# Performance work log

Hardware: AMD Instinct MI355X
Metric: run time of the kernel (lower is better)

The kernel has to match this reference:

```python
import jax, jax.numpy as jnp
import numpy as np

N, IN_F, OUT_F, H = 4096, 256, 64, 8

def setup_inputs() -> dict:
    key = jax.random.key(0)
    k1, k2, k3, k4 = jax.random.split(key, 4)
    x = jax.random.normal(k1, (N, IN_F), dtype=jnp.float32)
    adj = jax.random.randint(k2, (N, N), 0, 2, dtype=jnp.int32)
    # Xavier-uniform-ish init scale for params
    W = jax.random.uniform(k3, (H, IN_F, OUT_F), dtype=jnp.float32, minval=-1.0, maxval=1.0) * np.sqrt(6.0 / (IN_F + OUT_F))
    a = jax.random.uniform(k4, (H, 2 * OUT_F, 1), dtype=jnp.float32, minval=-1.0, maxval=1.0) * np.sqrt(6.0 / (2 * OUT_F + 1))
    return {"x": x, "adj": adj, "W": W, "a": a}

def reference(x, adj, W, a):
    # h: (H, N, F) per-head projected features
    h = jnp.einsum('nf,hfo->hno', x, W)
    F = h.shape[-1]
    # Decompose concat-score: [h_i || h_j] @ a == h_i @ a[:F] + h_j @ a[F:]
    a_src = a[:, :F, 0]   # (H, F)
    a_dst = a[:, F:, 0]   # (H, F)
    src = jnp.einsum('hno,ho->hn', h, a_src)  # (H, N)
    dst = jnp.einsum('hno,ho->hn', h, a_dst)  # (H, N)
    e = jax.nn.leaky_relu(src[:, :, None] + dst[:, None, :], negative_slope=0.2)  # (H, N, N)
    e = jnp.where(adj[None, :, :] == 0, -jnp.inf, e)
    alpha = jax.nn.softmax(e, axis=2)  # dropout is identity at eval
    h_prime = jnp.einsum('hnm,hmo->hno', alpha, h).mean(axis=0)  # (N, F)
    return jax.nn.elu(h_prime)
```

## Files before the change

kernel.cpp:

```cpp
#include <hip/hip_runtime.h>
#include <hip/hip_fp16.h>
#include <cstdint>

#define N_NODES 4096
#define IN_FEAT 256
#define OUT_FEAT 64
#define NHEAD 8
#define LOG2E 1.4426950408889634f

typedef _Float16 f16;
typedef f16   f16x2 __attribute__((ext_vector_type(2)));
typedef f16   f16x8 __attribute__((ext_vector_type(8)));
typedef float f32x4 __attribute__((ext_vector_type(4)));

#define OFF_SRCPK 4194304
#define OFF_DSTE1 4325376
#define OFF_DSTE5 4390912
#define OFF_EM    4718592
#define OFF_NUMA  21495808ULL
#define OFF_DENA  29884416ULL

union HU { unsigned u; f16x2 h; };
union A8 { f16x8 v; unsigned u[4]; };

__device__ __forceinline__ void async_copy16(const void* g, void* l) {
    __builtin_amdgcn_global_load_lds(
        (const __attribute__((address_space(1))) void*)g,
        (__attribute__((address_space(3))) void*)l, 16, 0, 0);
}

static __device__ inline unsigned pkh2(float a, float b) {
    union { f16 h[2]; unsigned u; } t;
    t.h[0] = (f16)a; t.h[1] = (f16)b; return t.u;
}

__global__ __launch_bounds__(256, 4) void gat_prep(
    const int*   __restrict__ adj,
    unsigned*    __restrict__ em32,
    float*       __restrict__ zeroBase,
    const float* __restrict__ x,
    const float* __restrict__ W,
    const float* __restrict__ a,
    f16*      __restrict__ h_t,
    unsigned* __restrict__ srcPK,
    f16*      __restrict__ dstE1,
    f16*      __restrict__ dstE5)
{
    __shared__ f16 xs[16][264];

    if (blockIdx.x >= 1536) {
        size_t off = ((size_t)(blockIdx.x - 1536) * 256 + threadIdx.x) * 8;
        float4 z = {0.f, 0.f, 0.f, 0.f};
        *(float4*)(zeroBase + off)     = z;
        *(float4*)(zeroBase + off + 4) = z;
        return;
    }
    if (blockIdx.x >= 512) {
        const int bi   = blockIdx.x - 512;
        const int wv   = threadIdx.x >> 6;
        const int lane = threadIdx.x & 63;
        const int row  = bi * 4 + wv;
        const int* p   = adj + (size_t)row * N_NODES;
        unsigned* dst  = em32 + (size_t)row * (N_NODES / 4);
        #pragma unroll 4
        for (int s = 0; s < 16; ++s) {
            int4 v = *(const int4*)(p + s * 256 + lane * 4);
            unsigned d = (v.x ? 0x000000FFu : 0u) | (v.y ? 0x0000FF00u : 0u)
                       | (v.z ? 0x00FF0000u : 0u) | (v.w ? 0xFF000000u : 0u);
            dst[s * 64 + lane] = d;
        }
        return;
    }

    const int lane = threadIdx.x & 63;
    const int wv   = threadIdx.x >> 6;
    const int tile = blockIdx.x >> 1;
    const int hd   = (blockIdx.x & 1) * 4 + wv;
    const int r    = lane & 15;
    const int q    = lane >> 4;
    const int nb   = tile * 16;

    #pragma unroll
    for (int c = 0; c < 4; ++c) {
        int idx = c * 1024 + threadIdx.x * 4;
        int row = idx >> 8, col = idx & 255;
        float4 v = *(const float4*)(x + (size_t)(nb + row) * IN_FEAT + col);
        uint2 st = { pkh2(v.x, v.y), pkh2(v.z, v.w) };
        *(uint2*)(&xs[row][col]) = st;
    }
    __syncthreads();

    const float* Wg = W + (size_t)hd * (IN_FEAT * OUT_FEAT);
    f32x4 acc[4] = {};

    #pragma unroll 2
    for (int k0 = 0; k0 < IN_FEAT; k0 += 32) {
        f16x8 af = *(const f16x8*)(&xs[r][k0 + q * 8]);
        #pragma unroll
        for (int f = 0; f < 4; ++f) {
            f16x8 bf;
            #pragma unroll
            for (int j = 0; j < 8; ++j)
                bf[j] = (f16)Wg[(size_t)(k0 + q * 8 + j) * OUT_FEAT + 16 * f + r];
            acc[f] = __builtin_amdgcn_mfma_f32_16x16x32_f16(af, bf, acc[f], 0, 0, 0);
        }
    }

    float asv[4], adv[4];
    #pragma unroll
    for (int f = 0; f < 4; ++f) {
        asv[f] = a[hd * 128 + 16 * f + r];
        adv[f] = a[hd * 128 + 64 + 16 * f + r];
    }
    float sp[4], dp[4];
    #pragma unroll
    for (int reg = 0; reg < 4; ++reg) {
        sp[reg] = acc[0][reg] * asv[0] + acc[1][reg] * asv[1]
                + acc[2][reg] * asv[2] + acc[3][reg] * asv[3];
        dp[reg] = acc[0][reg] * adv[0] + acc[1][reg] * adv[1]
                + acc[2][reg] * adv[2] + acc[3][reg] * adv[3];
    }
    #pragma unroll
    for (int m = 1; m <= 8; m <<= 1) {
        #pragma unroll
        for (int reg = 0; reg < 4; ++reg) {
            sp[reg] += __shfl_xor(sp[reg], m);
            dp[reg] += __shfl_xor(dp[reg], m);
        }
    }

    #pragma unroll
    for (int f = 0; f < 4; ++f) {
        uint2 st = { pkh2(acc[f][0], acc[f][1]), pkh2(acc[f][2], acc[f][3]) };
        *(uint2*)(h_t + (size_t)(hd * OUT_FEAT + 16 * f + r) * N_NODES + nb + 4 * q) = st;
    }

    if (r == 0) {
        #pragma unroll
        for (int reg = 0; reg < 4; ++reg) {
            int row = nb + 4 * q + reg;
            float s = sp[reg] * LOG2E;
            float d = dp[reg] * LOG2E;
            srcPK[hd * N_NODES + row] = pkh2(exp2f(s), exp2f(0.2f * s));
            dstE1[hd * N_NODES + row] = (f16)exp2f(d);
            dstE5[hd * N_NODES + row] = (f16)exp2f(0.2f * d);
        }
    }
}

__global__ __launch_bounds__(256, 4) void gat_phase2p(
    const f16* __restrict__ h_t,
    const unsigned* __restrict__ srcPK,
    const f16* __restrict__ dstE1,
    const f16* __restrict__ dstE5,
    const unsigned char* __restrict__ emask8,
    float* __restrict__ numA,
    float* __restrict__ denA)
{
    __shared__ f16 Vbuf[2][8320];

    const int t    = threadIdx.x;
    const int lane = t & 63;
    const int wv   = t >> 6;
    const int r    = lane & 15;
    const int q    = lane >> 4;
    const int q8   = q * 8;

    const int hd     = blockIdx.x >> 7;
    const int rowgrp = (blockIdx.x >> 2) & 31;
    const int chunk  = blockIdx.x & 3;
    const int nblk   = rowgrp * 128;
    const int n0     = nblk + wv * 32;
    const int mbase  = chunk * 1024;

    HU s0u, s1u;
    s0u.u = srcPK[hd * N_NODES + n0 + r];
    s1u.u = srcPK[hd * N_NODES + n0 + 16 + r];
    const f16x2 se1_0 = { s0u.h[0], s0u.h[0] };
    const f16x2 se5_0 = { s0u.h[1], s0u.h[1] };
    const f16x2 se1_1 = { s1u.h[0], s1u.h[0] };
    const f16x2 se5_1 = { s1u.h[1], s1u.h[1] };

    const f16* Vhead = h_t + (size_t)hd * OUT_FEAT * N_NODES + mbase;
    const f16* srcV  = Vhead + (size_t)(t >> 2) * N_NODES + (t & 3) * 8;
    const unsigned char* srcM =
        emask8 + (size_t)(nblk + (t >> 1)) * N_NODES + mbase + (t & 1) * 16;
    const f16* ebase = ((t >> 2) & 1) ? dstE5 : dstE1;
    const f16* esrc  = ebase + (size_t)hd * N_NODES + mbase
                             + (t >> 3) * 32 + (t & 3) * 8;

    f32x4 acc0 = {}, acc1 = {}, acc2 = {}, acc3 = {}, accD0 = {};
    f32x4 acc4 = {}, acc5 = {}, acc6 = {}, acc7 = {}, accD1 = {};
    f16x8 ones;
    #pragma unroll
    for (int j = 0; j < 8; ++j) ones[j] = (f16)1.0f;

    auto stage = [&](int buf, int it) {
        const int c64 = it * 64;
        async_copy16(srcV + c64,      &Vbuf[buf][t * 8]);
        async_copy16(srcV + c64 + 32, &Vbuf[buf][2048 + t * 8]);
        async_copy16(srcM + c64,      &Vbuf[buf][4096 + t * 8]);
        async_copy16(srcM + c64 + 32, &Vbuf[buf][6144 + t * 8]);
        if (t < 16) async_copy16(esrc + c64, &Vbuf[buf][8192 + t * 8]);
    };

    stage(0, 0);

    for (int it = 0; it < 16; ++it) {
        const int cur = it & 1;
        __syncthreads();

        stage(1 - cur, (it + 1) & 15);

        #pragma unroll
        for (int s = 0; s < 2; ++s) {
            const int vb = s * 2048;
            uint4 e1v = *(const uint4*)(&Vbuf[cur][8192 + s * 64 + q8]);
            uint4 e5v = *(const uint4*)(&Vbuf[cur][8224 + s * 64 + q8]);
            uint2 m0v = *(const uint2*)(&Vbuf[cur][4096 + s * 2048 + (wv * 32 + r) * 16 + q * 4]);
            uint2 m1v = *(const uint2*)(&Vbuf[cur][4096 + s * 2048 + (wv * 32 + 16 + r) * 16 + q * 4]);

            unsigned e1d[4] = {e1v.x, e1v.y, e1v.z, e1v.w};
            unsigned e5d[4] = {e5v.x, e5v.y, e5v.z, e5v.w};
            unsigned mk0[4], mk1[4];
            mk0[0] = __builtin_amdgcn_perm(0u, m0v.x, 0x01010000u);
            mk0[1] = __builtin_amdgcn_perm(0u, m0v.x, 0x03030202u);
            mk0[2] = __builtin_amdgcn_perm(0u, m0v.y, 0x01010000u);
            mk0[3] = __builtin_amdgcn_perm(0u, m0v.y, 0x03030202u);
            mk1[0] = __builtin_amdgcn_perm(0u, m1v.x, 0x01010000u);
            mk1[1] = __builtin_amdgcn_perm(0u, m1v.x, 0x03030202u);
            mk1[2] = __builtin_amdgcn_perm(0u, m1v.y, 0x01010000u);
            mk1[3] = __builtin_amdgcn_perm(0u, m1v.y, 0x03030202u);

            A8 A0, A1;
            #pragma unroll
            for (int jp = 0; jp < 4; ++jp) {
                HU ed1; ed1.u = e1d[jp];
                HU ed5; ed5.u = e5d[jp];
                HU w0, w1;
                w0.h = __builtin_elementwise_max(se1_0 * ed1.h, se5_0 * ed5.h);
                w1.h = __builtin_elementwise_max(se1_1 * ed1.h, se5_1 * ed5.h);
                A0.u[jp] = w0.u & mk0[jp];
                A1.u[jp] = w1.u & mk1[jp];
            }

            f16x8 b0 = *(const f16x8*)(&Vbuf[cur][vb + (     r) * 32 + q8]);
            f16x8 b1 = *(const f16x8*)(&Vbuf[cur][vb + (16 + r) * 32 + q8]);
            f16x8 b2 = *(const f16x8*)(&Vbuf[cur][vb + (32 + r) * 32 + q8]);
            f16x8 b3 = *(const f16x8*)(&Vbuf[cur][vb + (48 + r) * 32 + q8]);

            acc0  = __builtin_amdgcn_mfma_f32_16x16x32_f16(A0.v, b0,   acc0,  0, 0, 0);
            acc1  = __builtin_amdgcn_mfma_f32_16x16x32_f16(A0.v, b1,   acc1,  0, 0, 0);
            acc2  = __builtin_amdgcn_mfma_f32_16x16x32_f16(A0.v, b2,   acc2,  0, 0, 0);
            acc3  = __builtin_amdgcn_mfma_f32_16x16x32_f16(A0.v, b3,   acc3,  0, 0, 0);
            accD0 = __builtin_amdgcn_mfma_f32_16x16x32_f16(A0.v, ones, accD0, 0, 0, 0);
            acc4  = __builtin_amdgcn_mfma_f32_16x16x32_f16(A1.v, b0,   acc4,  0, 0, 0);
            acc5  = __builtin_amdgcn_mfma_f32_16x16x32_f16(A1.v, b1,   acc5,  0, 0, 0);
            acc6  = __builtin_amdgcn_mfma_f32_16x16x32_f16(A1.v, b2,   acc6,  0, 0, 0);
            acc7  = __builtin_amdgcn_mfma_f32_16x16x32_f16(A1.v, b3,   acc7,  0, 0, 0);
            accD1 = __builtin_amdgcn_mfma_f32_16x16x32_f16(A1.v, ones, accD1, 0, 0, 0);
        }
    }

    #pragma unroll
    for (int reg = 0; reg < 4; ++reg) {
        int row0 = n0 + 4 * q + reg;
        int row1 = row0 + 16;
        atomicAdd(&numA[((size_t)row0 * NHEAD + hd) * 64 +  0 + r], acc0[reg]);
        atomicAdd(&numA[((size_t)row0 * NHEAD + hd) * 64 + 16 + r], acc1[reg]);
        atomicAdd(&numA[((size_t)row0 * NHEAD + hd) * 64 + 32 + r], acc2[reg]);
        atomicAdd(&numA[((size_t)row0 * NHEAD + hd) * 64 + 48 + r], acc3[reg]);
        atomicAdd(&numA[((size_t)row1 * NHEAD + hd) * 64 +  0 + r], acc4[reg]);
        atomicAdd(&numA[((size_t)row1 * NHEAD + hd) * 64 + 16 + r], acc5[reg]);
        atomicAdd(&numA[((size_t)row1 * NHEAD + hd) * 64 + 32 + r], acc6[reg]);
        atomicAdd(&numA[((size_t)row1 * NHEAD + hd) * 64 + 48 + r], acc7[reg]);
        if (r == 0) {
            atomicAdd(&denA[(size_t)row0 * NHEAD + hd], accD0[reg]);
            atomicAdd(&denA[(size_t)row1 * NHEAD + hd], accD1[reg]);
        }
    }
}

__global__ __launch_bounds__(512) void gat_combine(
    const float* __restrict__ numA,
    const float* __restrict__ denA,
    float* __restrict__ out)
{
    int gid = blockIdx.x * 512 + threadIdx.x;
    int row = gid >> 5;
    int cp  = (gid & 31) * 2;
    float s0 = 0.f, s1 = 0.f;
    #pragma unroll
    for (int h = 0; h < NHEAD; ++h) {
        float2 v = *(const float2*)(numA + ((size_t)row * NHEAD + h) * 64 + cp);
        float inv = 1.f / denA[(size_t)row * NHEAD + h];
        s0 += v.x * inv;
        s1 += v.y * inv;
    }
    s0 *= 0.125f; s1 *= 0.125f;
    float e0 = s0 > 0.f ? s0 : expm1f(s0);
    float e1 = s1 > 0.f ? s1 : expm1f(s1);
    float2 pk = {e0, e1};
    *(float2*)(out + (size_t)row * OUT_FEAT + cp) = pk;
}

extern "C" void kernel_launch(void* const* d_in, const int* in_sizes, int n_in,
                              void* d_out, int out_size, void* d_ws, size_t ws_size,
                              hipStream_t stream)
{
    const float* x   = (const float*)d_in[0];
    const int*   adj = (const int*)d_in[1];
    const float* W   = (const float*)d_in[2];
    const float* a   = (const float*)d_in[3];
    float* out = (float*)d_out;

    char* ws = (char*)d_ws;
    f16*           h_t   = (f16*)ws;
    unsigned*      srcPK = (unsigned*)(ws + OFF_SRCPK);
    f16*           dstE1 = (f16*)(ws + OFF_DSTE1);
    f16*           dstE5 = (f16*)(ws + OFF_DSTE5);
    unsigned char* em    = (unsigned char*)(ws + OFF_EM);
    float*         numA  = (float*)(ws + OFF_NUMA);
    float*         denA  = (float*)(ws + OFF_DENA);

    gat_prep   <<<2576, 256, 0, stream>>>(adj, (unsigned*)em, numA,
                                          x, W, a, h_t, srcPK, dstE1, dstE5);
    gat_phase2p<<<1024, 256, 0, stream>>>(h_t, srcPK, dstE1, dstE5, em, numA, denA);
    gat_combine<<<256,  512, 0, stream>>>(numA, denA, out);
}
```

Before: 165.6 us.

## Replace atomic accumulation with per-chunk fp16 partials reduced in combine

Phase 2 no longer atomically adds into zeroed fp32 accumulators. Each of the four column chunks writes its own partial numerator, in fp16, and its own fp32 denominator, and the combine kernel sums the four partials. This drops the zero-fill blocks from the prep kernel and removes the atomic traffic. To keep the fp16 numerators in range, the exponentials are scaled by 2^-5; the scale cancels in the softmax ratio but costs some precision and adds extra partial-buffer reads in combine.

```diff
diff --git a/kernel.cpp b/kernel.cpp
--- a/kernel.cpp
+++ b/kernel.cpp
@@ -17,8 +17,8 @@
 #define OFF_DSTE1 4325376
 #define OFF_DSTE5 4390912
 #define OFF_EM    4718592
-#define OFF_NUMA  21495808ULL
-#define OFF_DENA  29884416ULL
+#define OFF_NUMP  21495808ULL
+#define OFF_DENP  38273024ULL
 
 union HU { unsigned u; f16x2 h; };
 union A8 { f16x8 v; unsigned u[4]; };
@@ -37,7 +37,6 @@
 __global__ __launch_bounds__(256, 4) void gat_prep(
     const int*   __restrict__ adj,
     unsigned*    __restrict__ em32,
-    float*       __restrict__ zeroBase,
     const float* __restrict__ x,
     const float* __restrict__ W,
     const float* __restrict__ a,
@@ -48,13 +47,6 @@
 {
     __shared__ f16 xs[16][264];
 
-    if (blockIdx.x >= 1536) {
-        size_t off = ((size_t)(blockIdx.x - 1536) * 256 + threadIdx.x) * 8;
-        float4 z = {0.f, 0.f, 0.f, 0.f};
-        *(float4*)(zeroBase + off)     = z;
-        *(float4*)(zeroBase + off + 4) = z;
-        return;
-    }
     if (blockIdx.x >= 512) {
         const int bi   = blockIdx.x - 512;
         const int wv   = threadIdx.x >> 6;
@@ -141,9 +133,9 @@
             int row = nb + 4 * q + reg;
             float s = sp[reg] * LOG2E;
             float d = dp[reg] * LOG2E;
-            srcPK[hd * N_NODES + row] = pkh2(exp2f(s), exp2f(0.2f * s));
-            dstE1[hd * N_NODES + row] = (f16)exp2f(d);
-            dstE5[hd * N_NODES + row] = (f16)exp2f(0.2f * d);
+            srcPK[hd * N_NODES + row] = pkh2(exp2f(s - 5.0f), exp2f(0.2f * s - 5.0f));
+            dstE1[hd * N_NODES + row] = (f16)exp2f(d - 5.0f);
+            dstE5[hd * N_NODES + row] = (f16)exp2f(0.2f * d - 5.0f);
         }
     }
 }
@@ -154,8 +146,8 @@
     const f16* __restrict__ dstE1,
     const f16* __restrict__ dstE5,
     const unsigned char* __restrict__ emask8,
-    float* __restrict__ numA,
-    float* __restrict__ denA)
+    f16*   __restrict__ numP,
+    float* __restrict__ denP)
 {
     __shared__ f16 Vbuf[2][8320];
 
@@ -262,28 +254,31 @@
         }
     }
 
+    const size_t cb = (size_t)chunk * N_NODES;
     #pragma unroll
     for (int reg = 0; reg < 4; ++reg) {
         int row0 = n0 + 4 * q + reg;
         int row1 = row0 + 16;
-        atomicAdd(&numA[((size_t)row0 * NHEAD + hd) * 64 +  0 + r], acc0[reg]);
-        atomicAdd(&numA[((size_t)row0 * NHEAD + hd) * 64 + 16 + r], acc1[reg]);
-        atomicAdd(&numA[((size_t)row0 * NHEAD + hd) * 64 + 32 + r], acc2[reg]);
-        atomicAdd(&numA[((size_t)row0 * NHEAD + hd) * 64 + 48 + r], acc3[reg]);
-        atomicAdd(&numA[((size_t)row1 * NHEAD + hd) * 64 +  0 + r], acc4[reg]);
-        atomicAdd(&numA[((size_t)row1 * NHEAD + hd) * 64 + 16 + r], acc5[reg]);
-        atomicAdd(&numA[((size_t)row1 * NHEAD + hd) * 64 + 32 + r], acc6[reg]);
-        atomicAdd(&numA[((size_t)row1 * NHEAD + hd) * 64 + 48 + r], acc7[reg]);
+        size_t b0 = ((cb + row0) * NHEAD + hd) * 64;
+        size_t b1 = ((cb + row1) * NHEAD + hd) * 64;
+        numP[b0 +      r] = (f16)acc0[reg];
+        numP[b0 + 16 + r] = (f16)acc1[reg];
+        numP[b0 + 32 + r] = (f16)acc2[reg];
+        numP[b0 + 48 + r] = (f16)acc3[reg];
+        numP[b1 +      r] = (f16)acc4[reg];
+        numP[b1 + 16 + r] = (f16)acc5[reg];
+        numP[b1 + 32 + r] = (f16)acc6[reg];
+        numP[b1 + 48 + r] = (f16)acc7[reg];
         if (r == 0) {
-            atomicAdd(&denA[(size_t)row0 * NHEAD + hd], accD0[reg]);
-            atomicAdd(&denA[(size_t)row1 * NHEAD + hd], accD1[reg]);
+            denP[(cb + row0) * NHEAD + hd] = accD0[reg];
+            denP[(cb + row1) * NHEAD + hd] = accD1[reg];
         }
     }
 }
 
 __global__ __launch_bounds__(512) void gat_combine(
-    const float* __restrict__ numA,
-    const float* __restrict__ denA,
+    const f16*   __restrict__ numP,
+    const float* __restrict__ denP,
     float* __restrict__ out)
 {
     int gid = blockIdx.x * 512 + threadIdx.x;
@@ -292,10 +287,18 @@
     float s0 = 0.f, s1 = 0.f;
     #pragma unroll
     for (int h = 0; h < NHEAD; ++h) {
-        float2 v = *(const float2*)(numA + ((size_t)row * NHEAD + h) * 64 + cp);
-        float inv = 1.f / denA[(size_t)row * NHEAD + h];
-        s0 += v.x * inv;
-        s1 += v.y * inv;
+        float n0 = 0.f, n1 = 0.f, den = 0.f;
+        #pragma unroll
+        for (int c = 0; c < 4; ++c) {
+            size_t base = ((size_t)c * N_NODES + row) * NHEAD + h;
+            HU u; u.u = *(const unsigned*)(numP + base * 64 + cp);
+            n0 += (float)u.h[0];
+            n1 += (float)u.h[1];
+            den += denP[base];
+        }
+        float inv = 1.f / den;
+        s0 += n0 * inv;
+        s1 += n1 * inv;
     }
     s0 *= 0.125f; s1 *= 0.125f;
     float e0 = s0 > 0.f ? s0 : expm1f(s0);
@@ -320,11 +323,11 @@
     f16*           dstE1 = (f16*)(ws + OFF_DSTE1);
     f16*           dstE5 = (f16*)(ws + OFF_DSTE5);
     unsigned char* em    = (unsigned char*)(ws + OFF_EM);
-    float*         numA  = (float*)(ws + OFF_NUMA);
-    float*         denA  = (float*)(ws + OFF_DENA);
-
-    gat_prep   <<<2576, 256, 0, stream>>>(adj, (unsigned*)em, numA,
+    f16*           numP  = (f16*)(ws + OFF_NUMP);
+    float*         denP  = (float*)(ws + OFF_DENP);
+
+    gat_prep   <<<1536, 256, 0, stream>>>(adj, (unsigned*)em,
                                           x, W, a, h_t, srcPK, dstE1, dstE5);
-    gat_phase2p<<<1024, 256, 0, stream>>>(h_t, srcPK, dstE1, dstE5, em, numA, denA);
-    gat_combine<<<256,  512, 0, stream>>>(numA, denA, out);
-}
+    gat_phase2p<<<1024, 256, 0, stream>>>(h_t, srcPK, dstE1, dstE5, em, numP, denP);
+    gat_combine<<<256,  512, 0, stream>>>(numP, denP, out);
+}
```

Result: faster. 145.4 us, median of 2 (-12.2%).
